# Performance work log

Measured on AMD Instinct MI355X. Metric: run time of the kernel, lower is better.

## Reference

```python
import jax, jax.numpy as jnp
import numpy as np

EPS = 1e-06


def setup_inputs() -> dict:
    key = jax.random.key(0)
    kq, kk, kv = jax.random.split(key, 3)
    B, H, T, P = 2, 8, 1024, 64
    Q = jax.random.normal(kq, (B, H, T, P), dtype=jnp.float32)
    K = jax.random.normal(kk, (B, H, T, P), dtype=jnp.float32)
    V = jax.random.normal(kv, (B, H, T, P), dtype=jnp.float32)
    return {"Q": Q, "K": K, "V": V}


def _scan_attention(Q, K, V):
    Q_feat = jnp.exp(Q)                                  # (B,H,T,P)
    K_feat = jnp.exp(K)                                  # (B,H,T,P)
    m0 = jnp.log(K_feat)                                 # (B,H,T,P)
    N0 = jnp.einsum('bhtp,bhtn->bhtpn', V, K_feat)       # (B,H,T,P,P) matrix state
    D0 = K_feat                                          # (B,H,T,P)

    def combine(x, y):
        m_x, N_x, D_x = x
        m_y, N_y, D_y = y
        m_new = jnp.maximum(m_x, m_y)
        scale_x = jnp.exp(m_x - m_new)
        scale_y = jnp.exp(m_y - m_new)
        N_new = N_x * scale_x[..., None] + N_y * scale_y[..., None]
        D_new = D_x * scale_x + D_y * scale_y
        return (m_new, N_new, D_new)

    m_cum, num_cum, denom_cum = jax.lax.associative_scan(combine, (m0, N0, D0), axis=2)

    Y_num = jnp.einsum('bhtp,bhtpq->bhtq', Q_feat, num_cum)   # (B,H,T,P)
    Y_den = jnp.einsum('bhtp,bhtp->bht', Q_feat, denom_cum)   # (B,H,T)
    Y = Y_num / (Y_den[..., None] + EPS)
    B, H, T, P = Q.shape
    return Y.transpose(0, 2, 1, 3).reshape(B, T, H * P)


def reference(Q, K, V):
    return _scan_attention(Q, K, V)
```

## Files before the change

### kernel.cpp

```cpp
#include <hip/hip_runtime.h>
#include <hip/hip_bf16.h>

#define TDIM 1024
#define PDIM 64
#define BHN  16
#define NCH  64
#define CHS  16

typedef __bf16 bf16_t;
typedef bf16_t bf16x8 __attribute__((ext_vector_type(8)));
typedef float  floatx4 __attribute__((ext_vector_type(4)));

__device__ __forceinline__ floatx4 mfma16(bf16x8 a, bf16x8 b, floatx4 c) {
    return __builtin_amdgcn_mfma_f32_16x16x32_bf16(a, b, c, 0, 0, 0);
}

__global__ __launch_bounds__(64) void scanfeat_kernel(
        const float* __restrict__ Q, const float* __restrict__ K,
        const float* __restrict__ V,
        bf16_t* __restrict__ W, bf16_t* __restrict__ U,
        bf16_t* __restrict__ Kft, float* __restrict__ den) {
    int g  = blockIdx.x;
    int bh = g & 15;
    int c  = g >> 4;
    int p  = threadIdx.x;
    size_t base = (size_t)bh * TDIM * PDIM;
    int t0 = c * CHS;

    float kq[CHS], qq_[CHS], vv[CHS];
#pragma unroll
    for (int i = 0; i < CHS; ++i) {
        kq[i]  = K[base + (size_t)(t0 + i) * PDIM + p];
        qq_[i] = Q[base + (size_t)(t0 + i) * PDIM + p];
        vv[i]  = V[base + (size_t)(t0 + i) * PDIM + p];
    }

    const float* Kb = K + base + p;
    float m0 = -INFINITY, m1 = -INFINITY, m2 = -INFINITY, m3 = -INFINITY;
    float s0 = 0.f, s1 = 0.f, s2 = 0.f, s3 = 0.f;
    int nrows = t0;
    int t = 0;
#pragma unroll 2
    for (; t + 4 <= nrows; t += 4) {
        float k0 = Kb[(size_t)(t + 0) * PDIM];
        float k1 = Kb[(size_t)(t + 1) * PDIM];
        float k2 = Kb[(size_t)(t + 2) * PDIM];
        float k3 = Kb[(size_t)(t + 3) * PDIM];
        m0 = fmaxf(m0, k0); m1 = fmaxf(m1, k1);
        m2 = fmaxf(m2, k2); m3 = fmaxf(m3, k3);
        float e0 = __expf(k0), e1 = __expf(k1);
        float e2 = __expf(k2), e3 = __expf(k3);
        s0 += e0 * e0; s1 += e1 * e1; s2 += e2 * e2; s3 += e3 * e3;
    }
    float m = fmaxf(fmaxf(m0, m1), fmaxf(m2, m3));
    float s = (s0 + s1) + (s2 + s3);

    __shared__ bf16_t ek_t[CHS][PDIM + 4];
    __shared__ float  dt[CHS][PDIM + 1];

#pragma unroll
    for (int i = 0; i < CHS; ++i) {
        int tg = t0 + i;
        m = fmaxf(m, kq[i]);
        float ek = __expf(kq[i]);
        s += ek * ek;
        float w = __expf(qq_[i] - m);
        W[base + (size_t)tg * PDIM + p] = (bf16_t)w;
        U[base + (size_t)tg * PDIM + p] = (bf16_t)(vv[i] * ek);
        ek_t[i][p] = (bf16_t)ek;
        dt[i][p] = w * s;
    }
    __syncthreads();

    {
        int tl = p >> 2, gg = p & 3;
        float d = 0.f;
#pragma unroll
        for (int i = 0; i < 16; ++i) d += dt[tl][i * 4 + gg];
        d += __shfl_xor(d, 1);
        d += __shfl_xor(d, 2);
        if (gg == 0) den[bh * TDIM + t0 + tl] = d;
    }

    {
        int hi = p >> 4, tl = p & 15;
#pragma unroll
        for (int it = 0; it < 16; ++it) {
            int q = it * 4 + hi;
            Kft[((size_t)bh * PDIM + q) * TDIM + t0 + tl] = ek_t[tl][q];
        }
    }
}

__global__ __launch_bounds__(512) void attn_kernel(
        const bf16_t* __restrict__ W, const bf16_t* __restrict__ U,
        const bf16_t* __restrict__ Kft, const float* __restrict__ den,
        float* __restrict__ out) {
    int bh  = blockIdx.x & 15;
    int i   = blockIdx.x >> 4;
    int tid = threadIdx.x;
    int wave = tid >> 6, lane = tid & 63;
    int lq = lane & 15, qd = lane >> 4;
    int sub = wave & 3;
    int par = wave >> 2;
    int b = bh >> 3, h = bh & 7;

    __shared__ bf16_t Wt[64][72];
    __shared__ bf16_t Ut[2][64][72];
    __shared__ bf16_t Kt[2][64][72];
    __shared__ __align__(16) char ctyraw[8 * 16 * 72 * 2];
    __shared__ float denb[64];
    bf16_t (*Ct)[16][72]  = (bf16_t (*)[16][72])ctyraw;
    float  (*Yred)[16][68] = (float (*)[16][68])ctyraw;

    size_t base = (size_t)bh * TDIM * PDIM;
    size_t kftb = (size_t)bh * PDIM * TDIM;
    int row = tid >> 3, c8 = (tid & 7) << 3;

    int4 wfrag = *(const int4*)(W + base + (size_t)(i * 64 + row) * PDIM + c8);
    int4 pu0 = *(const int4*)(U + base + (size_t)(0 * 64 + row) * PDIM + c8);
    int4 pk0 = *(const int4*)(Kft + kftb + (size_t)row * TDIM + 0 * 64 + c8);
    int4 pu1 = *(const int4*)(U + base + (size_t)(1 * 64 + row) * PDIM + c8);
    int4 pk1 = *(const int4*)(Kft + kftb + (size_t)row * TDIM + 1 * 64 + c8);
    *(int4*)&Wt[row][c8] = wfrag;
    if (tid < 64) denb[tid] = den[bh * TDIM + i * 64 + tid];
    __syncthreads();

    bf16x8 a0 = *(const bf16x8*)&Wt[sub * 16 + lq][qd * 8];
    bf16x8 a1 = *(const bf16x8*)&Wt[sub * 16 + lq][32 + qd * 8];

    floatx4 acc[4];
#pragma unroll
    for (int j = 0; j < 4; ++j) acc[j] = (floatx4){0.f, 0.f, 0.f, 0.f};

    int niter = (i >> 1) + 1;
    for (int kt2 = 0; kt2 < niter; ++kt2) {
        __syncthreads();
        *(int4*)&Ut[0][row][c8] = pu0;
        *(int4*)&Kt[0][row][c8] = pk0;
        *(int4*)&Ut[1][row][c8] = pu1;
        *(int4*)&Kt[1][row][c8] = pk1;
        if (kt2 + 1 < niter) {
            int ktn = 2 * kt2 + 2;
            int ktn1 = ktn + 1 > 15 ? 15 : ktn + 1;
            pu0 = *(const int4*)(U + base + (size_t)(ktn * 64 + row) * PDIM + c8);
            pk0 = *(const int4*)(Kft + kftb + (size_t)row * TDIM + ktn * 64 + c8);
            pu1 = *(const int4*)(U + base + (size_t)(ktn1 * 64 + row) * PDIM + c8);
            pk1 = *(const int4*)(Kft + kftb + (size_t)row * TDIM + ktn1 * 64 + c8);
        }
        __syncthreads();

        int kt = 2 * kt2 + par;
        if (kt <= i) {
            floatx4 cc[4];
#pragma unroll
            for (int j = 0; j < 4; ++j) {
                bf16x8 b0 = *(const bf16x8*)&Ut[par][j * 16 + lq][qd * 8];
                bf16x8 b1 = *(const bf16x8*)&Ut[par][j * 16 + lq][32 + qd * 8];
                floatx4 t = (floatx4){0.f, 0.f, 0.f, 0.f};
                t = mfma16(a0, b0, t);
                t = mfma16(a1, b1, t);
                cc[j] = t;
            }
            int trow0 = i * 64 + sub * 16;
#pragma unroll
            for (int j = 0; j < 4; ++j) {
#pragma unroll
                for (int r = 0; r < 4; ++r) {
                    float v = cc[j][r];
                    if (kt == i && (kt * 64 + j * 16 + lq) > (trow0 + qd * 4 + r))
                        v = 0.f;
                    Ct[wave][qd * 4 + r][j * 16 + lq] = (bf16_t)v;
                }
            }
            bf16x8 ca0 = *(const bf16x8*)&Ct[wave][lq][qd * 8];
            bf16x8 ca1 = *(const bf16x8*)&Ct[wave][lq][32 + qd * 8];
#pragma unroll
            for (int j = 0; j < 4; ++j) {
                bf16x8 kb0 = *(const bf16x8*)&Kt[par][j * 16 + lq][qd * 8];
                bf16x8 kb1 = *(const bf16x8*)&Kt[par][j * 16 + lq][32 + qd * 8];
                acc[j] = mfma16(ca0, kb0, acc[j]);
                acc[j] = mfma16(ca1, kb1, acc[j]);
            }
        }
    }

    __syncthreads();
    if (par == 1) {
#pragma unroll
        for (int j = 0; j < 4; ++j)
#pragma unroll
            for (int r = 0; r < 4; ++r)
                Yred[sub][qd * 4 + r][j * 16 + lq] = acc[j][r];
    }
    __syncthreads();
    if (par == 0) {
#pragma unroll
        for (int j = 0; j < 4; ++j) {
#pragma unroll
            for (int r = 0; r < 4; ++r) {
                int trow_l = sub * 16 + qd * 4 + r;
                int tg = i * 64 + trow_l;
                float y = acc[j][r] + Yred[sub][qd * 4 + r][j * 16 + lq];
                y = y / (denb[trow_l] + 1e-6f);
                out[((size_t)b * TDIM + tg) * (8 * PDIM) + h * PDIM + j * 16 + lq] = y;
            }
        }
    }
}

extern "C" void kernel_launch(void* const* d_in, const int* in_sizes, int n_in,
                              void* d_out, int out_size, void* d_ws, size_t ws_size,
                              hipStream_t stream) {
    const float* Q = (const float*)d_in[0];
    const float* K = (const float*)d_in[1];
    const float* V = (const float*)d_in[2];
    float* out = (float*)d_out;

    bf16_t* Wf   = (bf16_t*)d_ws;
    bf16_t* Uf   = Wf + (size_t)BHN * TDIM * PDIM;
    bf16_t* Kft  = Uf + (size_t)BHN * TDIM * PDIM;
    float*  den  = (float*)(Kft + (size_t)BHN * TDIM * PDIM);

    scanfeat_kernel<<<BHN * NCH, 64, 0, stream>>>(Q, K, V, Wf, Uf, Kft, den);
    attn_kernel<<<256, 512, 0, stream>>>(Wf, Uf, Kft, den, out);
}
```

Before: 101.8 us.

## Fuse feature computation into attention kernel and precompute per-chunk K stats

The separate feature kernel that wrote bf16 W, U and transposed K features to workspace is replaced by a small stats kernel that stores per-8-row chunk max and sum of exp(2K). The attention kernel then combines prefix stats, computes W and the denominator in-block, and builds exp(K) and V*exp(K) tiles on the fly from fp32 K/V with an LDS transpose. This removes the quadratic prefix rescan and the intermediate global round-trips. In exchange, exp(K) is recomputed for every query block, fp32 loads are twice as wide as bf16, and the transposed LDS stores may cause bank conflicts.

```diff
diff --git a/kernel.cpp b/kernel.cpp
--- a/kernel.cpp
+++ b/kernel.cpp
@@ -4,8 +4,8 @@
 #define TDIM 1024
 #define PDIM 64
 #define BHN  16
-#define NCH  64
-#define CHS  16
+#define SCH  8
+#define NSC  128
 
 typedef __bf16 bf16_t;
 typedef bf16_t bf16x8 __attribute__((ext_vector_type(8)));
@@ -15,86 +15,28 @@
     return __builtin_amdgcn_mfma_f32_16x16x32_bf16(a, b, c, 0, 0, 0);
 }
 
-__global__ __launch_bounds__(64) void scanfeat_kernel(
+__global__ __launch_bounds__(64) void stats_kernel(
+        const float* __restrict__ K, float2* __restrict__ stats) {
+    int bh = blockIdx.x >> 7;
+    int c  = blockIdx.x & 127;
+    int p  = threadIdx.x;
+    const float* Kb = K + (size_t)bh * TDIM * PDIM + (size_t)c * SCH * PDIM + p;
+    float k[SCH];
+#pragma unroll
+    for (int i = 0; i < SCH; ++i) k[i] = Kb[i * PDIM];
+    float m = -INFINITY, s = 0.f;
+#pragma unroll
+    for (int i = 0; i < SCH; ++i) {
+        m = fmaxf(m, k[i]);
+        float e = __expf(k[i]);
+        s += e * e;
+    }
+    stats[((size_t)(bh << 7) + c) * PDIM + p] = make_float2(m, s);
+}
+
+__global__ __launch_bounds__(512) void featattn_kernel(
         const float* __restrict__ Q, const float* __restrict__ K,
-        const float* __restrict__ V,
-        bf16_t* __restrict__ W, bf16_t* __restrict__ U,
-        bf16_t* __restrict__ Kft, float* __restrict__ den) {
-    int g  = blockIdx.x;
-    int bh = g & 15;
-    int c  = g >> 4;
-    int p  = threadIdx.x;
-    size_t base = (size_t)bh * TDIM * PDIM;
-    int t0 = c * CHS;
-
-    float kq[CHS], qq_[CHS], vv[CHS];
-#pragma unroll
-    for (int i = 0; i < CHS; ++i) {
-        kq[i]  = K[base + (size_t)(t0 + i) * PDIM + p];
-        qq_[i] = Q[base + (size_t)(t0 + i) * PDIM + p];
-        vv[i]  = V[base + (size_t)(t0 + i) * PDIM + p];
-    }
-
-    const float* Kb = K + base + p;
-    float m0 = -INFINITY, m1 = -INFINITY, m2 = -INFINITY, m3 = -INFINITY;
-    float s0 = 0.f, s1 = 0.f, s2 = 0.f, s3 = 0.f;
-    int nrows = t0;
-    int t = 0;
-#pragma unroll 2
-    for (; t + 4 <= nrows; t += 4) {
-        float k0 = Kb[(size_t)(t + 0) * PDIM];
-        float k1 = Kb[(size_t)(t + 1) * PDIM];
-        float k2 = Kb[(size_t)(t + 2) * PDIM];
-        float k3 = Kb[(size_t)(t + 3) * PDIM];
-        m0 = fmaxf(m0, k0); m1 = fmaxf(m1, k1);
-        m2 = fmaxf(m2, k2); m3 = fmaxf(m3, k3);
-        float e0 = __expf(k0), e1 = __expf(k1);
-        float e2 = __expf(k2), e3 = __expf(k3);
-        s0 += e0 * e0; s1 += e1 * e1; s2 += e2 * e2; s3 += e3 * e3;
-    }
-    float m = fmaxf(fmaxf(m0, m1), fmaxf(m2, m3));
-    float s = (s0 + s1) + (s2 + s3);
-
-    __shared__ bf16_t ek_t[CHS][PDIM + 4];
-    __shared__ float  dt[CHS][PDIM + 1];
-
-#pragma unroll
-    for (int i = 0; i < CHS; ++i) {
-        int tg = t0 + i;
-        m = fmaxf(m, kq[i]);
-        float ek = __expf(kq[i]);
-        s += ek * ek;
-        float w = __expf(qq_[i] - m);
-        W[base + (size_t)tg * PDIM + p] = (bf16_t)w;
-        U[base + (size_t)tg * PDIM + p] = (bf16_t)(vv[i] * ek);
-        ek_t[i][p] = (bf16_t)ek;
-        dt[i][p] = w * s;
-    }
-    __syncthreads();
-
-    {
-        int tl = p >> 2, gg = p & 3;
-        float d = 0.f;
-#pragma unroll
-        for (int i = 0; i < 16; ++i) d += dt[tl][i * 4 + gg];
-        d += __shfl_xor(d, 1);
-        d += __shfl_xor(d, 2);
-        if (gg == 0) den[bh * TDIM + t0 + tl] = d;
-    }
-
-    {
-        int hi = p >> 4, tl = p & 15;
-#pragma unroll
-        for (int it = 0; it < 16; ++it) {
-            int q = it * 4 + hi;
-            Kft[((size_t)bh * PDIM + q) * TDIM + t0 + tl] = ek_t[tl][q];
-        }
-    }
-}
-
-__global__ __launch_bounds__(512) void attn_kernel(
-        const bf16_t* __restrict__ W, const bf16_t* __restrict__ U,
-        const bf16_t* __restrict__ Kft, const float* __restrict__ den,
+        const float* __restrict__ V, const float2* __restrict__ stats,
         float* __restrict__ out) {
     int bh  = blockIdx.x & 15;
     int i   = blockIdx.x >> 4;
@@ -114,16 +56,63 @@
     float  (*Yred)[16][68] = (float (*)[16][68])ctyraw;
 
     size_t base = (size_t)bh * TDIM * PDIM;
-    size_t kftb = (size_t)bh * PDIM * TDIM;
-    int row = tid >> 3, c8 = (tid & 7) << 3;
-
-    int4 wfrag = *(const int4*)(W + base + (size_t)(i * 64 + row) * PDIM + c8);
-    int4 pu0 = *(const int4*)(U + base + (size_t)(0 * 64 + row) * PDIM + c8);
-    int4 pk0 = *(const int4*)(Kft + kftb + (size_t)row * TDIM + 0 * 64 + c8);
-    int4 pu1 = *(const int4*)(U + base + (size_t)(1 * 64 + row) * PDIM + c8);
-    int4 pk1 = *(const int4*)(Kft + kftb + (size_t)row * TDIM + 1 * 64 + c8);
-    *(int4*)&Wt[row][c8] = wfrag;
-    if (tid < 64) denb[tid] = den[bh * TDIM + i * 64 + tid];
+    int trow = tid >> 3;
+    int c0   = (tid & 7) << 3;
+
+    const float* Kst = K + base + (size_t)trow * PDIM + c0;
+    const float* Vst = V + base + (size_t)trow * PDIM + c0;
+    floatx4 pk0a = *(const floatx4*)(Kst);
+    floatx4 pk0b = *(const floatx4*)(Kst + 4);
+    floatx4 pv0a = *(const floatx4*)(Vst);
+    floatx4 pv0b = *(const floatx4*)(Vst + 4);
+    floatx4 pk1a = *(const floatx4*)(Kst + 64 * PDIM);
+    floatx4 pk1b = *(const floatx4*)(Kst + 64 * PDIM + 4);
+    floatx4 pv1a = *(const floatx4*)(Vst + 64 * PDIM);
+    floatx4 pv1b = *(const floatx4*)(Vst + 64 * PDIM + 4);
+
+    {
+        int gchunk = 8 * i + wave;
+        const float2* st2 = stats + (size_t)(bh << 7) * PDIM + lane;
+        float m0 = -INFINITY, m1 = -INFINITY, m2 = -INFINITY, m3 = -INFINITY;
+        float s0 = 0.f, s1 = 0.f, s2 = 0.f, s3 = 0.f;
+        int cc = 0;
+        for (; cc + 4 <= gchunk; cc += 4) {
+            float2 v0 = st2[(size_t)(cc + 0) * PDIM];
+            float2 v1 = st2[(size_t)(cc + 1) * PDIM];
+            float2 v2 = st2[(size_t)(cc + 2) * PDIM];
+            float2 v3 = st2[(size_t)(cc + 3) * PDIM];
+            m0 = fmaxf(m0, v0.x); s0 += v0.y;
+            m1 = fmaxf(m1, v1.x); s1 += v1.y;
+            m2 = fmaxf(m2, v2.x); s2 += v2.y;
+            m3 = fmaxf(m3, v3.x); s3 += v3.y;
+        }
+        for (; cc < gchunk; ++cc) {
+            float2 v = st2[(size_t)cc * PDIM];
+            m0 = fmaxf(m0, v.x); s0 += v.y;
+        }
+        float m = fmaxf(fmaxf(m0, m1), fmaxf(m2, m3));
+        float s = (s0 + s1) + (s2 + s3);
+
+        int t0 = i * 64 + wave * 8;
+        float kr[8], qr[8];
+#pragma unroll
+        for (int j = 0; j < 8; ++j) {
+            kr[j] = K[base + (size_t)(t0 + j) * PDIM + lane];
+            qr[j] = Q[base + (size_t)(t0 + j) * PDIM + lane];
+        }
+#pragma unroll
+        for (int j = 0; j < 8; ++j) {
+            m = fmaxf(m, kr[j]);
+            float e = __expf(kr[j]);
+            s += e * e;
+            float wv = __expf(qr[j] - m);
+            Wt[wave * 8 + j][lane] = (bf16_t)wv;
+            float d = wv * s;
+#pragma unroll
+            for (int off = 32; off > 0; off >>= 1) d += __shfl_xor(d, off);
+            if (lane == 0) denb[wave * 8 + j] = d;
+        }
+    }
     __syncthreads();
 
     bf16x8 a0 = *(const bf16x8*)&Wt[sub * 16 + lq][qd * 8];
@@ -136,23 +125,55 @@
     int niter = (i >> 1) + 1;
     for (int kt2 = 0; kt2 < niter; ++kt2) {
         __syncthreads();
-        *(int4*)&Ut[0][row][c8] = pu0;
-        *(int4*)&Kt[0][row][c8] = pk0;
-        *(int4*)&Ut[1][row][c8] = pu1;
-        *(int4*)&Kt[1][row][c8] = pk1;
+        {
+            float kk[8] = {pk0a.x, pk0a.y, pk0a.z, pk0a.w,
+                           pk0b.x, pk0b.y, pk0b.z, pk0b.w};
+            float vv[8] = {pv0a.x, pv0a.y, pv0a.z, pv0a.w,
+                           pv0b.x, pv0b.y, pv0b.z, pv0b.w};
+            bf16x8 uv, kv;
+#pragma unroll
+            for (int j = 0; j < 8; ++j) {
+                float e = __expf(kk[j]);
+                kv[j] = (bf16_t)e;
+                uv[j] = (bf16_t)(vv[j] * e);
+            }
+            *(bf16x8*)&Ut[0][trow][c0] = uv;
+#pragma unroll
+            for (int j = 0; j < 8; ++j) Kt[0][c0 + j][trow] = kv[j];
+        }
+        {
+            float kk[8] = {pk1a.x, pk1a.y, pk1a.z, pk1a.w,
+                           pk1b.x, pk1b.y, pk1b.z, pk1b.w};
+            float vv[8] = {pv1a.x, pv1a.y, pv1a.z, pv1a.w,
+                           pv1b.x, pv1b.y, pv1b.z, pv1b.w};
+            bf16x8 uv, kv;
+#pragma unroll
+            for (int j = 0; j < 8; ++j) {
+                float e = __expf(kk[j]);
+                kv[j] = (bf16_t)e;
+                uv[j] = (bf16_t)(vv[j] * e);
+            }
+            *(bf16x8*)&Ut[1][trow][c0] = uv;
+#pragma unroll
+            for (int j = 0; j < 8; ++j) Kt[1][c0 + j][trow] = kv[j];
+        }
         if (kt2 + 1 < niter) {
-            int ktn = 2 * kt2 + 2;
-            int ktn1 = ktn + 1 > 15 ? 15 : ktn + 1;
-            pu0 = *(const int4*)(U + base + (size_t)(ktn * 64 + row) * PDIM + c8);
-            pk0 = *(const int4*)(Kft + kftb + (size_t)row * TDIM + ktn * 64 + c8);
-            pu1 = *(const int4*)(U + base + (size_t)(ktn1 * 64 + row) * PDIM + c8);
-            pk1 = *(const int4*)(Kft + kftb + (size_t)row * TDIM + ktn1 * 64 + c8);
+            const float* Kn = Kst + (size_t)(2 * kt2 + 2) * 64 * PDIM;
+            const float* Vn = Vst + (size_t)(2 * kt2 + 2) * 64 * PDIM;
+            pk0a = *(const floatx4*)(Kn);
+            pk0b = *(const floatx4*)(Kn + 4);
+            pv0a = *(const floatx4*)(Vn);
+            pv0b = *(const floatx4*)(Vn + 4);
+            pk1a = *(const floatx4*)(Kn + 64 * PDIM);
+            pk1b = *(const floatx4*)(Kn + 64 * PDIM + 4);
+            pv1a = *(const floatx4*)(Vn + 64 * PDIM);
+            pv1b = *(const floatx4*)(Vn + 64 * PDIM + 4);
         }
         __syncthreads();
 
         int kt = 2 * kt2 + par;
         if (kt <= i) {
-            floatx4 cc[4];
+            floatx4 cc4[4];
 #pragma unroll
             for (int j = 0; j < 4; ++j) {
                 bf16x8 b0 = *(const bf16x8*)&Ut[par][j * 16 + lq][qd * 8];
@@ -160,14 +181,14 @@
                 floatx4 t = (floatx4){0.f, 0.f, 0.f, 0.f};
                 t = mfma16(a0, b0, t);
                 t = mfma16(a1, b1, t);
-                cc[j] = t;
+                cc4[j] = t;
             }
             int trow0 = i * 64 + sub * 16;
 #pragma unroll
             for (int j = 0; j < 4; ++j) {
 #pragma unroll
                 for (int r = 0; r < 4; ++r) {
-                    float v = cc[j][r];
+                    float v = cc4[j][r];
                     if (kt == i && (kt * 64 + j * 16 + lq) > (trow0 + qd * 4 + r))
                         v = 0.f;
                     Ct[wave][qd * 4 + r][j * 16 + lq] = (bf16_t)v;
@@ -217,11 +238,8 @@
     const float* V = (const float*)d_in[2];
     float* out = (float*)d_out;
 
-    bf16_t* Wf   = (bf16_t*)d_ws;
-    bf16_t* Uf   = Wf + (size_t)BHN * TDIM * PDIM;
-    bf16_t* Kft  = Uf + (size_t)BHN * TDIM * PDIM;
-    float*  den  = (float*)(Kft + (size_t)BHN * TDIM * PDIM);
-
-    scanfeat_kernel<<<BHN * NCH, 64, 0, stream>>>(Q, K, V, Wf, Uf, Kft, den);
-    attn_kernel<<<256, 512, 0, stream>>>(Wf, Uf, Kft, den, out);
-}
+    float2* stats = (float2*)d_ws;
+
+    stats_kernel<<<BHN * NSC, 64, 0, stream>>>(K, stats);
+    featattn_kernel<<<256, 512, 0, stream>>>(Q, K, V, stats, out);
+}
```

Measured after the change: 95.64 us. 6.0% less time.
